# Kernel tuning notes

Measured on AMD Instinct MI355X. Metric: run time of the kernel, lower is better.

Reference implementation:

```python
import jax, jax.numpy as jnp
import numpy as np

B, T, C, HS = 4, 4096, 1024, 128

def setup_inputs() -> dict:
    key = jax.random.key(0)
    kx, kq, kk, kv = jax.random.split(key, 4)
    x = jax.random.normal(kx, (B, T, C), dtype=jnp.float32)
    # bias-free Linear weights, stored as (in, out) so projection is x @ W
    scale = 1.0 / np.sqrt(C)
    Wq = jax.random.normal(kq, (C, HS), dtype=jnp.float32) * scale
    Wk = jax.random.normal(kk, (C, HS), dtype=jnp.float32) * scale
    Wv = jax.random.normal(kv, (C, HS), dtype=jnp.float32) * scale
    return {"x": x, "Wq": Wq, "Wk": Wk, "Wv": Wv}

def reference(x, Wq, Wk, Wv):
    # x: (B,T,C) -> q,k,v: (B,T,HS)
    q = jnp.einsum('btc,ch->bth', x, Wq)
    k = jnp.einsum('btc,ch->bth', x, Wk)
    v = jnp.einsum('btc,ch->bth', x, Wv)
    hs = k.shape[-1]
    # scaled scores (B,T,T) with causal mask
    wei = jnp.einsum('bth,bsh->bts', q, k) * (hs ** -0.5)
    causal = jnp.tril(jnp.ones((q.shape[1], q.shape[1]), dtype=bool))
    wei = jnp.where(causal, wei, -jnp.inf)
    wei = jax.nn.softmax(wei, axis=-1)
    # dropout p=0.0 -> identity
    out = jnp.einsum('bts,bsh->bth', wei, v)
    return out
```

## Files before the change

kernel.cpp:

```cpp
#include <hip/hip_runtime.h>
#include <hip/hip_bf16.h>

typedef __attribute__((ext_vector_type(8))) short short8;
typedef __attribute__((ext_vector_type(4))) short s4v;
typedef __attribute__((ext_vector_type(4))) float f32x4;

#define BATCH 4
#define TLEN 4096
#define CDIM 1024
#define HSD 128
#define MROWS (BATCH*TLEN)

#define QSCALE 0.12751744f

#ifdef __HIP_DEVICE_COMPILE__
  #define MFMA16(a,b,c) __builtin_amdgcn_mfma_f32_16x16x16bf16_1k(a,b,c,0,0,0)
#else
  #define MFMA16(a,b,c) (c)
#endif

__device__ __forceinline__ unsigned short f2bf(float f){
    unsigned u = __builtin_bit_cast(unsigned, f);
    u = (u + 0x7FFFu + ((u >> 16) & 1u)) >> 16;
    return (unsigned short)u;
}
__device__ __forceinline__ unsigned pkbf(float a, float b){
    unsigned ua = (__builtin_bit_cast(unsigned, a) + 0x8000u) >> 16;
    unsigned ub = (__builtin_bit_cast(unsigned, b) + 0x8000u) & 0xFFFF0000u;
    return ua | ub;
}

__global__ void prep_w_k(const float* __restrict__ Wq, const float* __restrict__ Wk,
                         const float* __restrict__ Wv, unsigned short* __restrict__ Wt){
    __shared__ float tile[32][33];
    const int w = blockIdx.z;
    const float* W = (w == 0) ? Wq : ((w == 1) ? Wk : Wv);
    const int c0 = blockIdx.x * 32, h0 = blockIdx.y * 32;
    const int lx = threadIdx.x & 31, ly = threadIdx.x >> 5;
#pragma unroll
    for (int i = 0; i < 4; i++){
        int c = c0 + ly + i * 8;
        tile[ly + i * 8][lx] = W[(size_t)c * HSD + h0 + lx];
    }
    __syncthreads();
#pragma unroll
    for (int i = 0; i < 4; i++){
        int h = h0 + ly + i * 8;
        Wt[((size_t)w * HSD + h) * CDIM + c0 + lx] = f2bf(tile[lx][ly + i * 8]);
    }
}

__device__ __forceinline__ void stage_wb(unsigned short* buf, const unsigned short* g, int tid){
#pragma unroll
    for (int i = 0; i < 3; i++){
        int c = i * 512 + tid;
        int row = c >> 2, kp = c & 3;
        int swz = (row & 3) ^ ((row >> 2) & 3);
        const unsigned short* gp = g + (size_t)row * CDIM + ((kp ^ swz) << 3);
        unsigned short* lp = buf + (c << 3);
        __builtin_amdgcn_global_load_lds((const __attribute__((address_space(1))) void*)gp,
                                         (__attribute__((address_space(3))) void*)lp, 16, 0, 0);
    }
}

__global__ __launch_bounds__(512) void proj_k(const float* __restrict__ x,
                                              const unsigned short* __restrict__ Wt,
                                              unsigned short* __restrict__ Qb,
                                              unsigned short* __restrict__ Kb,
                                              unsigned short* __restrict__ Vt){
    __shared__ unsigned short As[2][64 * 32];
    __shared__ unsigned short Bs[2][384 * 32];

    const int tid = threadIdx.x, lane = tid & 63, wave = tid >> 6;
    const int m = lane & 15, quad = lane >> 4;
    const int wr = wave & 1;
    const int wc = wave >> 1;
    const int rb = blockIdx.x * 64;

    const float* gA = x + (size_t)rb * CDIM;

    const int arow = tid >> 2, ach = tid & 3;
    const int aswz = (arow & 3) ^ ((arow >> 2) & 3);
    const int agc = ach ^ aswz;
    const float* agp = gA + (size_t)arow * CDIM + (agc << 3);

    f32x4 acc[6][2];
#pragma unroll
    for (int i = 0; i < 6; i++)
#pragma unroll
        for (int j = 0; j < 2; j++) acc[i][j] = (f32x4)0.f;

    stage_wb(&Bs[0][0], Wt, tid);
    if (tid < 256){
        float4 a0 = *(const float4*)(agp);
        float4 a1 = *(const float4*)(agp + 4);
        short8 o;
        o[0]=(short)f2bf(a0.x); o[1]=(short)f2bf(a0.y); o[2]=(short)f2bf(a0.z); o[3]=(short)f2bf(a0.w);
        o[4]=(short)f2bf(a1.x); o[5]=(short)f2bf(a1.y); o[6]=(short)f2bf(a1.z); o[7]=(short)f2bf(a1.w);
        *(short8*)&As[0][arow * 32 + (ach << 3)] = o;
    }
    __syncthreads();

    int cur = 0;
    for (int kc = 0; kc < CDIM / 32; ++kc){
        float4 a0n, a1n;
        if (kc + 1 < CDIM / 32){
            stage_wb(&Bs[cur ^ 1][0], Wt + (kc + 1) * 32, tid);
            if (tid < 256){
                a0n = *(const float4*)(agp + (kc + 1) * 32);
                a1n = *(const float4*)(agp + (kc + 1) * 32 + 4);
            }
        }
        {
            short8 aF[6], bF[2];
#pragma unroll
            for (int i = 0; i < 6; i++){
                int ra = wc * 96 + i * 16 + m;
                int sa = (ra & 3) ^ ((ra >> 2) & 3);
                aF[i] = *(const short8*)&Bs[cur][ra * 32 + ((quad ^ sa) << 3)];
            }
#pragma unroll
            for (int j = 0; j < 2; j++){
                int rn = wr * 32 + j * 16 + m;
                int sb = (rn & 3) ^ ((rn >> 2) & 3);
                bF[j] = *(const short8*)&As[cur][rn * 32 + ((quad ^ sb) << 3)];
            }
#pragma unroll
            for (int i = 0; i < 6; i++)
#pragma unroll
                for (int j = 0; j < 2; j++)
                    acc[i][j] = __builtin_amdgcn_mfma_f32_16x16x32_bf16(aF[i], bF[j], acc[i][j], 0, 0, 0);
        }
        if (kc + 1 < CDIM / 32 && tid < 256){
            short8 o;
            o[0]=(short)f2bf(a0n.x); o[1]=(short)f2bf(a0n.y); o[2]=(short)f2bf(a0n.z); o[3]=(short)f2bf(a0n.w);
            o[4]=(short)f2bf(a1n.x); o[5]=(short)f2bf(a1n.y); o[6]=(short)f2bf(a1n.z); o[7]=(short)f2bf(a1n.w);
            *(short8*)&As[cur ^ 1][arow * 32 + (ach << 3)] = o;
        }
        __syncthreads();
        cur ^= 1;
    }

    const int b = rb >> 12;
#pragma unroll
    for (int i = 0; i < 6; i++){
        const int hbase = wc * 96 + i * 16;
        const int type = hbase >> 7;
        const int hp = hbase + quad * 4;
#pragma unroll
        for (int j = 0; j < 2; j++){
            const int t = rb + wr * 32 + j * 16 + m;
            if (type == 0){
                ushort4 v;
                v.x = f2bf(acc[i][j][0] * QSCALE); v.y = f2bf(acc[i][j][1] * QSCALE);
                v.z = f2bf(acc[i][j][2] * QSCALE); v.w = f2bf(acc[i][j][3] * QSCALE);
                *(ushort4*)(Qb + (size_t)t * HSD + hp) = v;
            } else if (type == 1){
                ushort4 v;
                v.x = f2bf(acc[i][j][0]); v.y = f2bf(acc[i][j][1]);
                v.z = f2bf(acc[i][j][2]); v.w = f2bf(acc[i][j][3]);
                *(ushort4*)(Kb + (size_t)t * HSD + (hp - 128)) = v;
            } else {
                const int tt = t & (TLEN - 1);
#pragma unroll
                for (int r = 0; r < 4; r++)
                    Vt[((size_t)b * HSD + (hp - 256 + r)) * TLEN + tt] = f2bf(acc[i][j][r]);
            }
        }
    }
}

__device__ __forceinline__ void stage_k_tile(unsigned short* buf, const unsigned short* g,
                                             int tid){
#pragma unroll
    for (int i = 0; i < 2; i++){
        int slot = i * 512 + tid;
        int row = slot >> 4;
        int ch  = slot & 15;
        const unsigned short* gp = g + row * 128 + ((ch ^ (row & 15)) << 3);
        unsigned short* lp = buf + (slot << 3);
        __builtin_amdgcn_global_load_lds((const __attribute__((address_space(1))) void*)gp,
                                         (__attribute__((address_space(3))) void*)lp, 16, 0, 0);
    }
}
__device__ __forceinline__ void stage_v_tile(unsigned short* buf, const unsigned short* g,
                                             int tid){
#pragma unroll
    for (int i = 0; i < 2; i++){
        int slot = i * 512 + tid;
        int row = slot >> 3;
        int ch  = slot & 7;
        const unsigned short* gp = g + (size_t)row * TLEN + ((ch ^ (row & 7)) << 3);
        unsigned short* lp = buf + (slot << 3);
        __builtin_amdgcn_global_load_lds((const __attribute__((address_space(1))) void*)gp,
                                         (__attribute__((address_space(3))) void*)lp, 16, 0, 0);
    }
}

__global__ __launch_bounds__(512) void attn_k(const unsigned short* __restrict__ Qb,
                       const unsigned short* __restrict__ Kb,
                       const unsigned short* __restrict__ Vts,
                       float* __restrict__ Opart, float* __restrict__ lpart, int seglen){
    __shared__ unsigned short Kt[2][64 * 128];
    __shared__ unsigned short Vs[2][128 * 64];

    const int tid = threadIdx.x, lane = tid & 63, wave = tid >> 6;
    const int m = lane & 15, quad = lane >> 4;
    const int q0 = ((int)gridDim.x - 1 - (int)blockIdx.x) * 128;
    const int seg = blockIdx.y, b = blockIdx.z;
    const int g0 = seg * seglen;
    if (g0 >= q0 + 128) return;
    const int gend = min(g0 + seglen, q0 + 128);
    const int nT = (gend - g0) >> 6;

    const int q0w = q0 + wave * 16;
    const size_t rowg = (size_t)b * TLEN + q0w;

    const unsigned short* kbase = Kb + (size_t)b * TLEN * HSD;
    const unsigned short* vbase = Vts + (size_t)b * HSD * TLEN;

    short8 aQ[4];
#pragma unroll
    for (int kk = 0; kk < 4; kk++)
        aQ[kk] = *(const short8*)(Qb + (rowg + m) * HSD + kk * 32 + quad * 8);

    stage_k_tile(&Kt[0][0], kbase + (size_t)g0 * HSD, tid);
    stage_v_tile(&Vs[0][0], vbase + g0, tid);

    f32x4 accO[8];
#pragma unroll
    for (int i = 0; i < 8; i++) accO[i] = (f32x4)0.f;
    float lp = 0.f;

    asm volatile("s_waitcnt vmcnt(0)" ::: "memory");
#pragma unroll
    for (int kk = 0; kk < 4; kk++){
        f32x4 q_ = __builtin_bit_cast(f32x4, aQ[kk]);
        asm volatile("" : "+v"(q_));
        aQ[kk] = __builtin_bit_cast(short8, q_);
    }

    int cur = 0;
    for (int t = 0; t < nT; ++t){
        const int s0 = g0 + t * 64;
        if (t + 1 < nT){
            stage_k_tile(&Kt[cur ^ 1][0], kbase + (size_t)(s0 + 64) * HSD, tid);
            stage_v_tile(&Vs[cur ^ 1][0], vbase + (s0 + 64), tid);
            asm volatile("s_waitcnt vmcnt(4)" ::: "memory");
        } else {
            asm volatile("s_waitcnt vmcnt(0)" ::: "memory");
        }
        __builtin_amdgcn_s_barrier();
        __builtin_amdgcn_sched_barrier(0);
        if (s0 <= q0w + 15){
            const unsigned short* Ktc = &Kt[cur][0];
            const unsigned short* Vsc = &Vs[cur][0];
            f32x4 S[4];
            __builtin_amdgcn_s_setprio(1);
#pragma unroll
            for (int ns = 0; ns < 4; ns++){
                f32x4 sa = (f32x4)0.f;
#pragma unroll
                for (int kk = 0; kk < 4; kk++){
                    short8 bK = *(const short8*)&Ktc[(ns * 16 + m) * 128 + (((kk * 4 + quad) ^ m) << 3)];
                    sa = __builtin_amdgcn_mfma_f32_16x16x32_bf16(bK, aQ[kk], sa, 0, 0, 0);
                }
                S[ns] = sa;
            }
            __builtin_amdgcn_s_setprio(0);
            if (s0 + 63 > q0w){
                int qg = q0w + m;
#pragma unroll
                for (int ns = 0; ns < 4; ns++){
#pragma unroll
                    for (int r = 0; r < 4; r++){
                        int sg = s0 + ns * 16 + quad * 4 + r;
                        if (sg > qg) S[ns][r] = -1e30f;
                    }
                }
            }
            s4v aP[4];
#pragma unroll
            for (int ns = 0; ns < 4; ns++){
                float p0 = exp2f(S[ns][0]), p1 = exp2f(S[ns][1]);
                float p2 = exp2f(S[ns][2]), p3 = exp2f(S[ns][3]);
                lp += (p0 + p1) + (p2 + p3);
                uint2 u;
                u.x = pkbf(p0, p1);
                u.y = pkbf(p2, p3);
                aP[ns] = __builtin_bit_cast(s4v, u);
            }
            __builtin_amdgcn_s_setprio(1);
#pragma unroll
            for (int sub = 0; sub < 8; sub++){
#pragma unroll
                for (int ns = 0; ns < 4; ns++){
                    s4v bV = *(const s4v*)&Vsc[(sub * 16 + m) * 64 +
                            (((2 * ns + (quad >> 1)) ^ (m & 7)) << 3) + (quad & 1) * 4];
                    accO[sub] = MFMA16(aP[ns], bV, accO[sub]);
                }
            }
            __builtin_amdgcn_s_setprio(0);
        }
        __builtin_amdgcn_sched_barrier(0);
        __builtin_amdgcn_s_barrier();
        cur ^= 1;
    }
    lp += __shfl_xor(lp, 16, 64);
    lp += __shfl_xor(lp, 32, 64);
    if (quad == 0)
        lpart[(size_t)seg * MROWS + rowg + m] = lp;
    float* ob = Opart + (size_t)seg * MROWS * HSD;
#pragma unroll
    for (int sub = 0; sub < 8; sub++)
#pragma unroll
        for (int r = 0; r < 4; r++)
            ob[(rowg + quad * 4 + r) * HSD + sub * 16 + m] = accO[sub][r];
}

__global__ void merge_k(const float* __restrict__ Opart, const float* __restrict__ lpart,
                        float* __restrict__ out, int nseg, int seglen){
    int idx = blockIdx.x * 256 + threadIdx.x;
    int row = idx >> 7;
    int t = row & (TLEN - 1);
    int q0 = t & ~127;
    int nsv = min(nseg, (q0 + 127) / seglen + 1);
    float L = 0.f, o = 0.f;
    for (int s = 0; s < nsv; s++){
        L += lpart[(size_t)s * MROWS + row];
        o += Opart[(size_t)s * MROWS * HSD + idx];
    }
    out[idx] = o / L;
}

extern "C" void kernel_launch(void* const* d_in, const int* in_sizes, int n_in,
                              void* d_out, int out_size, void* d_ws, size_t ws_size,
                              hipStream_t stream) {
    const float* x  = (const float*)d_in[0];
    const float* Wq = (const float*)d_in[1];
    const float* Wk = (const float*)d_in[2];
    const float* Wv = (const float*)d_in[3];
    float* out = (float*)d_out;
    char* w = (char*)d_ws;

    unsigned short* Wt = (unsigned short*)w;
    unsigned short* Qb = (unsigned short*)(w + ((size_t)1u  << 20));
    unsigned short* Kb = (unsigned short*)(w + ((size_t)5u  << 20));
    unsigned short* Vt = (unsigned short*)(w + ((size_t)9u  << 20));
    float* lpart       = (float*)(w + ((size_t)13u << 20));
    float* Opart;
    int nseg;
    const size_t segbytes = (size_t)MROWS * HSD * 4;
    if (ws_size >= ((size_t)14u << 20) + 8 * segbytes){
        nseg = 8;  Opart = (float*)(w + ((size_t)14u << 20));
    } else if (ws_size >= ((size_t)14u << 20) + 4 * segbytes){
        nseg = 4;  Opart = (float*)(w + ((size_t)14u << 20));
    } else {
        nseg = 1;  Opart = out;
    }
    const int seglen = TLEN / nseg;

    prep_w_k<<<dim3(CDIM / 32, HSD / 32, 3), 256, 0, stream>>>(Wq, Wk, Wv, Wt);
    proj_k<<<dim3(MROWS / 64), 512, 0, stream>>>(x, Wt, Qb, Kb, Vt);
    attn_k<<<dim3(TLEN / 128, nseg, BATCH), 512, 0, stream>>>(Qb, Kb, Vt, Opart, lpart, seglen);
    merge_k<<<(MROWS * HSD) / 256, 256, 0, stream>>>(Opart, lpart, out, nseg, seglen);
}
```

Baseline: 200.5 us.

## Give each attention wave two query tiles and pipeline projection A-loads across all threads

The attention kernel now runs 256 threads (4 waves) per block, and each wave handles 32 query rows as two 16-row tiles. Every K and V fragment read from LDS is therefore reused for two MFMAs, which halves LDS traffic per unit of work. The cost is roughly double the accumulator registers, and a launch bound of 2 blocks per CU is added to keep occupancy. The projection kernel now has all 512 threads load 4 floats each instead of 256 threads loading 8, and replaces __syncthreads with an explicit vmcnt wait plus barrier so the next tile's loads overlap the MFMAs.

```diff
diff --git a/kernel.cpp b/kernel.cpp
--- a/kernel.cpp
+++ b/kernel.cpp
@@ -79,10 +79,11 @@
 
     const float* gA = x + (size_t)rb * CDIM;
 
-    const int arow = tid >> 2, ach = tid & 3;
-    const int aswz = (arow & 3) ^ ((arow >> 2) & 3);
-    const int agc = ach ^ aswz;
-    const float* agp = gA + (size_t)arow * CDIM + (agc << 3);
+    const int arow = tid >> 3, ach = tid & 7;
+    const int asw = (arow & 3) ^ ((arow >> 2) & 3);
+    const float* agp = gA + (size_t)arow * CDIM + ((((ach >> 1) ^ asw) << 3) + (ach & 1) * 4);
+    unsigned short* asp0 = &As[0][arow * 32 + (ach << 2)];
+    unsigned short* asp1 = &As[1][arow * 32 + (ach << 2)];
 
     f32x4 acc[6][2];
 #pragma unroll
@@ -91,26 +92,26 @@
         for (int j = 0; j < 2; j++) acc[i][j] = (f32x4)0.f;
 
     stage_wb(&Bs[0][0], Wt, tid);
-    if (tid < 256){
+    {
         float4 a0 = *(const float4*)(agp);
-        float4 a1 = *(const float4*)(agp + 4);
-        short8 o;
-        o[0]=(short)f2bf(a0.x); o[1]=(short)f2bf(a0.y); o[2]=(short)f2bf(a0.z); o[3]=(short)f2bf(a0.w);
-        o[4]=(short)f2bf(a1.x); o[5]=(short)f2bf(a1.y); o[6]=(short)f2bf(a1.z); o[7]=(short)f2bf(a1.w);
-        *(short8*)&As[0][arow * 32 + (ach << 3)] = o;
+        ushort4 o;
+        o.x = f2bf(a0.x); o.y = f2bf(a0.y); o.z = f2bf(a0.z); o.w = f2bf(a0.w);
+        *(ushort4*)asp0 = o;
     }
     __syncthreads();
 
     int cur = 0;
     for (int kc = 0; kc < CDIM / 32; ++kc){
-        float4 a0n, a1n;
+        float4 a0n;
         if (kc + 1 < CDIM / 32){
+            a0n = *(const float4*)(agp + (kc + 1) * 32);
             stage_wb(&Bs[cur ^ 1][0], Wt + (kc + 1) * 32, tid);
-            if (tid < 256){
-                a0n = *(const float4*)(agp + (kc + 1) * 32);
-                a1n = *(const float4*)(agp + (kc + 1) * 32 + 4);
-            }
-        }
+            asm volatile("s_waitcnt vmcnt(4)" ::: "memory");
+        } else {
+            asm volatile("s_waitcnt vmcnt(0)" ::: "memory");
+        }
+        __builtin_amdgcn_s_barrier();
+        __builtin_amdgcn_sched_barrier(0);
         {
             short8 aF[6], bF[2];
 #pragma unroll
@@ -131,15 +132,14 @@
                 for (int j = 0; j < 2; j++)
                     acc[i][j] = __builtin_amdgcn_mfma_f32_16x16x32_bf16(aF[i], bF[j], acc[i][j], 0, 0, 0);
         }
-        if (kc + 1 < CDIM / 32 && tid < 256){
-            short8 o;
-            o[0]=(short)f2bf(a0n.x); o[1]=(short)f2bf(a0n.y); o[2]=(short)f2bf(a0n.z); o[3]=(short)f2bf(a0n.w);
-            o[4]=(short)f2bf(a1n.x); o[5]=(short)f2bf(a1n.y); o[6]=(short)f2bf(a1n.z); o[7]=(short)f2bf(a1n.w);
-            *(short8*)&As[cur ^ 1][arow * 32 + (ach << 3)] = o;
-        }
-        __syncthreads();
+        if (kc + 1 < CDIM / 32){
+            ushort4 o;
+            o.x = f2bf(a0n.x); o.y = f2bf(a0n.y); o.z = f2bf(a0n.z); o.w = f2bf(a0n.w);
+            *(ushort4*)((cur == 0) ? asp1 : asp0) = o;
+        }
         cur ^= 1;
     }
+    __builtin_amdgcn_s_barrier();
 
     const int b = rb >> 12;
 #pragma unroll
@@ -173,8 +173,8 @@
 __device__ __forceinline__ void stage_k_tile(unsigned short* buf, const unsigned short* g,
                                              int tid){
 #pragma unroll
-    for (int i = 0; i < 2; i++){
-        int slot = i * 512 + tid;
+    for (int i = 0; i < 4; i++){
+        int slot = i * 256 + tid;
         int row = slot >> 4;
         int ch  = slot & 15;
         const unsigned short* gp = g + row * 128 + ((ch ^ (row & 15)) << 3);
@@ -186,8 +186,8 @@
 __device__ __forceinline__ void stage_v_tile(unsigned short* buf, const unsigned short* g,
                                              int tid){
 #pragma unroll
-    for (int i = 0; i < 2; i++){
-        int slot = i * 512 + tid;
+    for (int i = 0; i < 4; i++){
+        int slot = i * 256 + tid;
         int row = slot >> 3;
         int ch  = slot & 7;
         const unsigned short* gp = g + (size_t)row * TLEN + ((ch ^ (row & 7)) << 3);
@@ -197,7 +197,7 @@
     }
 }
 
-__global__ __launch_bounds__(512) void attn_k(const unsigned short* __restrict__ Qb,
+__global__ __launch_bounds__(256, 2) void attn_k(const unsigned short* __restrict__ Qb,
                        const unsigned short* __restrict__ Kb,
                        const unsigned short* __restrict__ Vts,
                        float* __restrict__ Opart, float* __restrict__ lpart, int seglen){
@@ -213,31 +213,37 @@
     const int gend = min(g0 + seglen, q0 + 128);
     const int nT = (gend - g0) >> 6;
 
-    const int q0w = q0 + wave * 16;
+    const int q0w = q0 + wave * 32;
     const size_t rowg = (size_t)b * TLEN + q0w;
 
     const unsigned short* kbase = Kb + (size_t)b * TLEN * HSD;
     const unsigned short* vbase = Vts + (size_t)b * HSD * TLEN;
 
-    short8 aQ[4];
-#pragma unroll
-    for (int kk = 0; kk < 4; kk++)
-        aQ[kk] = *(const short8*)(Qb + (rowg + m) * HSD + kk * 32 + quad * 8);
+    short8 aQ[2][4];
+#pragma unroll
+    for (int jq = 0; jq < 2; jq++)
+#pragma unroll
+        for (int kk = 0; kk < 4; kk++)
+            aQ[jq][kk] = *(const short8*)(Qb + (rowg + jq * 16 + m) * HSD + kk * 32 + quad * 8);
 
     stage_k_tile(&Kt[0][0], kbase + (size_t)g0 * HSD, tid);
     stage_v_tile(&Vs[0][0], vbase + g0, tid);
 
-    f32x4 accO[8];
-#pragma unroll
-    for (int i = 0; i < 8; i++) accO[i] = (f32x4)0.f;
-    float lp = 0.f;
+    f32x4 accO[2][8];
+#pragma unroll
+    for (int jq = 0; jq < 2; jq++)
+#pragma unroll
+        for (int i = 0; i < 8; i++) accO[jq][i] = (f32x4)0.f;
+    float lp0 = 0.f, lp1 = 0.f;
 
     asm volatile("s_waitcnt vmcnt(0)" ::: "memory");
 #pragma unroll
+    for (int jq = 0; jq < 2; jq++)
+#pragma unroll
     for (int kk = 0; kk < 4; kk++){
-        f32x4 q_ = __builtin_bit_cast(f32x4, aQ[kk]);
+        f32x4 q_ = __builtin_bit_cast(f32x4, aQ[jq][kk]);
         asm volatile("" : "+v"(q_));
-        aQ[kk] = __builtin_bit_cast(short8, q_);
+        aQ[jq][kk] = __builtin_bit_cast(short8, q_);
     }
 
     int cur = 0;
@@ -246,49 +252,54 @@
         if (t + 1 < nT){
             stage_k_tile(&Kt[cur ^ 1][0], kbase + (size_t)(s0 + 64) * HSD, tid);
             stage_v_tile(&Vs[cur ^ 1][0], vbase + (s0 + 64), tid);
-            asm volatile("s_waitcnt vmcnt(4)" ::: "memory");
+            asm volatile("s_waitcnt vmcnt(8)" ::: "memory");
         } else {
             asm volatile("s_waitcnt vmcnt(0)" ::: "memory");
         }
         __builtin_amdgcn_s_barrier();
         __builtin_amdgcn_sched_barrier(0);
-        if (s0 <= q0w + 15){
+        if (s0 <= q0w + 31){
             const unsigned short* Ktc = &Kt[cur][0];
             const unsigned short* Vsc = &Vs[cur][0];
-            f32x4 S[4];
+            f32x4 S0[4], S1[4];
             __builtin_amdgcn_s_setprio(1);
 #pragma unroll
             for (int ns = 0; ns < 4; ns++){
-                f32x4 sa = (f32x4)0.f;
+                f32x4 sa0 = (f32x4)0.f, sa1 = (f32x4)0.f;
 #pragma unroll
                 for (int kk = 0; kk < 4; kk++){
                     short8 bK = *(const short8*)&Ktc[(ns * 16 + m) * 128 + (((kk * 4 + quad) ^ m) << 3)];
-                    sa = __builtin_amdgcn_mfma_f32_16x16x32_bf16(bK, aQ[kk], sa, 0, 0, 0);
+                    sa0 = __builtin_amdgcn_mfma_f32_16x16x32_bf16(bK, aQ[0][kk], sa0, 0, 0, 0);
+                    sa1 = __builtin_amdgcn_mfma_f32_16x16x32_bf16(bK, aQ[1][kk], sa1, 0, 0, 0);
                 }
-                S[ns] = sa;
+                S0[ns] = sa0; S1[ns] = sa1;
             }
             __builtin_amdgcn_s_setprio(0);
             if (s0 + 63 > q0w){
-                int qg = q0w + m;
+                int qg0 = q0w + m, qg1 = q0w + 16 + m;
 #pragma unroll
                 for (int ns = 0; ns < 4; ns++){
 #pragma unroll
                     for (int r = 0; r < 4; r++){
                         int sg = s0 + ns * 16 + quad * 4 + r;
-                        if (sg > qg) S[ns][r] = -1e30f;
+                        if (sg > qg0) S0[ns][r] = -1e30f;
+                        if (sg > qg1) S1[ns][r] = -1e30f;
                     }
                 }
             }
-            s4v aP[4];
+            s4v aP0[4], aP1[4];
 #pragma unroll
             for (int ns = 0; ns < 4; ns++){
-                float p0 = exp2f(S[ns][0]), p1 = exp2f(S[ns][1]);
-                float p2 = exp2f(S[ns][2]), p3 = exp2f(S[ns][3]);
-                lp += (p0 + p1) + (p2 + p3);
-                uint2 u;
-                u.x = pkbf(p0, p1);
-                u.y = pkbf(p2, p3);
-                aP[ns] = __builtin_bit_cast(s4v, u);
+                float p0 = exp2f(S0[ns][0]), p1 = exp2f(S0[ns][1]);
+                float p2 = exp2f(S0[ns][2]), p3 = exp2f(S0[ns][3]);
+                lp0 += (p0 + p1) + (p2 + p3);
+                uint2 u; u.x = pkbf(p0, p1); u.y = pkbf(p2, p3);
+                aP0[ns] = __builtin_bit_cast(s4v, u);
+                float r0 = exp2f(S1[ns][0]), r1 = exp2f(S1[ns][1]);
+                float r2 = exp2f(S1[ns][2]), r3 = exp2f(S1[ns][3]);
+                lp1 += (r0 + r1) + (r2 + r3);
+                uint2 w; w.x = pkbf(r0, r1); w.y = pkbf(r2, r3);
+                aP1[ns] = __builtin_bit_cast(s4v, w);
             }
             __builtin_amdgcn_s_setprio(1);
 #pragma unroll
@@ -297,7 +308,8 @@
                 for (int ns = 0; ns < 4; ns++){
                     s4v bV = *(const s4v*)&Vsc[(sub * 16 + m) * 64 +
                             (((2 * ns + (quad >> 1)) ^ (m & 7)) << 3) + (quad & 1) * 4];
-                    accO[sub] = MFMA16(aP[ns], bV, accO[sub]);
+                    accO[0][sub] = MFMA16(aP0[ns], bV, accO[0][sub]);
+                    accO[1][sub] = MFMA16(aP1[ns], bV, accO[1][sub]);
                 }
             }
             __builtin_amdgcn_s_setprio(0);
@@ -306,16 +318,22 @@
         __builtin_amdgcn_s_barrier();
         cur ^= 1;
     }
-    lp += __shfl_xor(lp, 16, 64);
-    lp += __shfl_xor(lp, 32, 64);
-    if (quad == 0)
-        lpart[(size_t)seg * MROWS + rowg + m] = lp;
+    lp0 += __shfl_xor(lp0, 16, 64);
+    lp0 += __shfl_xor(lp0, 32, 64);
+    lp1 += __shfl_xor(lp1, 16, 64);
+    lp1 += __shfl_xor(lp1, 32, 64);
+    if (quad == 0){
+        lpart[(size_t)seg * MROWS + rowg + m] = lp0;
+        lpart[(size_t)seg * MROWS + rowg + 16 + m] = lp1;
+    }
     float* ob = Opart + (size_t)seg * MROWS * HSD;
 #pragma unroll
+    for (int jq = 0; jq < 2; jq++)
+#pragma unroll
     for (int sub = 0; sub < 8; sub++)
 #pragma unroll
         for (int r = 0; r < 4; r++)
-            ob[(rowg + quad * 4 + r) * HSD + sub * 16 + m] = accO[sub][r];
+            ob[(rowg + jq * 16 + quad * 4 + r) * HSD + sub * 16 + m] = accO[jq][sub][r];
 }
 
 __global__ void merge_k(const float* __restrict__ Opart, const float* __restrict__ lpart,
@@ -362,6 +380,6 @@
 
     prep_w_k<<<dim3(CDIM / 32, HSD / 32, 3), 256, 0, stream>>>(Wq, Wk, Wv, Wt);
     proj_k<<<dim3(MROWS / 64), 512, 0, stream>>>(x, Wt, Qb, Kb, Vt);
-    attn_k<<<dim3(TLEN / 128, nseg, BATCH), 512, 0, stream>>>(Qb, Kb, Vt, Opart, lpart, seglen);
+    attn_k<<<dim3(TLEN / 128, nseg, BATCH), 256, 0, stream>>>(Qb, Kb, Vt, Opart, lpart, seglen);
     merge_k<<<(MROWS * HSD) / 256, 256, 0, stream>>>(Opart, lpart, out, nseg, seglen);
 }
```

Measured after the change: 193.2 us. -3.6%, faster.
